# Kernel tuning notes

Measured on AMD Instinct MI355X. Metric: run time of the kernel, lower is better.

## Reference

```python
import jax, jax.numpy as jnp
import numpy as np

N, C, H, M = 4096, 1024, 16, 4096
D = C // H
EPS = 1e-6


def rms_norm(x, g):
    # RMSNorm32: normalize in fp32 with eps=1e-6, affine scale g
    x32 = x.astype(jnp.float32)
    inv = jax.lax.rsqrt(jnp.mean(x32 * x32, axis=-1, keepdims=True) + EPS)
    return (x32 * inv).astype(x.dtype) * g


def setup_inputs() -> dict:
    key = jax.random.key(0)
    ks = jax.random.split(key, 6)
    s = 1.0 / np.sqrt(C)
    return {
        "x": jax.random.normal(ks[0], (N, C), jnp.float32),
        "g1": jnp.ones((C,), jnp.float32),
        "g2": jnp.ones((C,), jnp.float32),
        "w_qkv": jax.random.normal(ks[1], (C, 3 * C), jnp.float32) * s,
        "w_o": jax.random.normal(ks[2], (C, C), jnp.float32) * s,
        "w1": jax.random.normal(ks[3], (C, M), jnp.float32) * s,
        "w2": jax.random.normal(ks[4], (M, C), jnp.float32) * (1.0 / np.sqrt(M)),
    }


def reference(x, g1, g2, w_qkv, w_o, w1, w2):
    # --- pre-norm + full multi-head self-attention over all N sparse tokens ---
    h = rms_norm(x, g1)                                   # [N, C]
    qkv = (h @ w_qkv).reshape(N, 3, H, D)                 # [N, 3, H, D]
    q, k, v = qkv[:, 0], qkv[:, 1], qkv[:, 2]             # [N, H, D]
    scale = 1.0 / np.sqrt(D)
    scores = jnp.einsum('nhd,mhd->hnm', q, k) * scale     # [H, N, N]
    attn = jax.nn.softmax(scores, axis=-1)
    o = jnp.einsum('hnm,mhd->nhd', attn, v).reshape(N, C) # [N, C]
    x = x + o @ w_o                                       # residual
    # --- pre-norm + gated-free MLP (GELU tanh) ---
    h2 = rms_norm(x, g2)
    m = jax.nn.gelu(h2 @ w1, approximate=True) @ w2       # [N, C]
    return x + m
```

## Files before the change

### kernel.cpp

```cpp
#include <hip/hip_runtime.h>
#include <stdint.h>

#define TOK 4096
#define CH  1024
#define NH  16
#define HD  64
#define FF  4096

typedef __attribute__((ext_vector_type(8))) short bf16x8;
typedef __attribute__((ext_vector_type(4))) float f32x4;
typedef __attribute__((ext_vector_type(16))) float f32x16;

__device__ __forceinline__ unsigned short f2bf(float f) {
    union { float f; unsigned u; } v; v.f = f;
    unsigned u = v.u;
    u += 0x7fffu + ((u >> 16) & 1u);
    return (unsigned short)(u >> 16);
}

__device__ __forceinline__ unsigned cvtpk(float a, float b) {
    unsigned r;
    asm("v_cvt_pk_bf16_f32 %0, %1, %2" : "=v"(r) : "v"(a), "v"(b));
    return r;
}

__device__ __forceinline__ void load_lds16(const void* g, void* l) {
    __builtin_amdgcn_global_load_lds(
        (const __attribute__((address_space(1))) unsigned int*)g,
        (__attribute__((address_space(3))) unsigned int*)l, 16, 0, 0);
}

__device__ __forceinline__ float gelu_tanh(float u) {
    float z = 0.7978845608028654f * (u + 0.044715f * u * u * u);
    float e = __expf(2.0f * z);
    return 0.5f * u * (1.0f + (1.0f - 2.0f / (e + 1.0f)));
}

__global__ __launch_bounds__(256) void wT_kernel(const float* __restrict__ in,
                                                 unsigned short* __restrict__ out,
                                                 int K, int Nn) {
    __shared__ float tile[32][33];
    int k0 = blockIdx.x * 32, n0 = blockIdx.y * 32;
    int t = threadIdx.x, r = t >> 3, c = t & 7;
#pragma unroll
    for (int i = 0; i < 4; i++)
        tile[r][c + 8 * i] = in[(size_t)(k0 + r) * Nn + n0 + c + 8 * i];
    __syncthreads();
#pragma unroll
    for (int i = 0; i < 4; i++)
        out[(size_t)(n0 + r) * K + k0 + c + 8 * i] = f2bf(tile[c + 8 * i][r]);
}

__global__ __launch_bounds__(256) void rms_kernel(const float* __restrict__ x,
                                                  const float* __restrict__ g,
                                                  unsigned short* __restrict__ out) {
    int row = blockIdx.x, t = threadIdx.x;
    const float4* xr = (const float4*)(x + (size_t)row * CH);
    float4 v = xr[t];
    float ss = v.x * v.x + v.y * v.y + v.z * v.z + v.w * v.w;
#pragma unroll
    for (int m = 32; m; m >>= 1) ss += __shfl_xor(ss, m, 64);
    __shared__ float wsum[4];
    if ((t & 63) == 0) wsum[t >> 6] = ss;
    __syncthreads();
    float inv = rsqrtf((wsum[0] + wsum[1] + wsum[2] + wsum[3]) * (1.0f / CH) + 1e-6f);
    float4 gv = ((const float4*)g)[t];
    ushort4 o;
    o.x = f2bf(v.x * inv * gv.x);
    o.y = f2bf(v.y * inv * gv.y);
    o.z = f2bf(v.z * inv * gv.z);
    o.w = f2bf(v.w * inv * gv.w);
    ((ushort4*)(out + (size_t)row * CH))[t] = o;
}

template<int BM, int BN, int EPI>
__global__ __launch_bounds__(256) void gemm_bt(const unsigned short* __restrict__ A,
                                               const unsigned short* __restrict__ Bt,
                                               void* __restrict__ outp,
                                               const float* __restrict__ resid,
                                               int M, int Nn, int K) {
    __shared__ __align__(16) unsigned short ldsA[2][BM * 32];
    __shared__ __align__(16) unsigned short ldsB[2][BN * 32];
    const int t = threadIdx.x, l = t & 63, w = t >> 6;
    const int nbn = Nn / BN;
    const int bid = blockIdx.x, nwg = gridDim.x, cpx = nwg >> 3;
    const int swz = (bid & 7) * cpx + (bid >> 3);
    const int bm = swz / nbn, bn = swz % nbn;
    const int wr = w >> 1, wc = w & 1;
    constexpr int MF = BM / 32, NF = BN / 32;
    const unsigned short* Ag = A + (size_t)bm * BM * K;
    const unsigned short* Bg = Bt + (size_t)bn * BN * K;

    f32x4 acc[MF][NF];
#pragma unroll
    for (int m = 0; m < MF; m++)
#pragma unroll
        for (int n = 0; n < NF; n++) acc[m][n] = {0.f, 0.f, 0.f, 0.f};

    auto stage = [&](int buf, int kt) {
#pragma unroll
        for (int p = 0; p < BM / 64; p++) {
            int c = t + 256 * p;
            load_lds16(Ag + (size_t)(c >> 2) * K + kt * 32 + (c & 3) * 8, &ldsA[buf][c * 8]);
        }
#pragma unroll
        for (int p = 0; p < BN / 64; p++) {
            int c = t + 256 * p;
            load_lds16(Bg + (size_t)(c >> 2) * K + kt * 32 + (c & 3) * 8, &ldsB[buf][c * 8]);
        }
    };

    stage(0, 0);
    __syncthreads();
    const int nkt = K >> 5;
    for (int kt = 0; kt < nkt; kt++) {
        const int buf = kt & 1;
        if (kt + 1 < nkt) stage(buf ^ 1, kt + 1);
        bf16x8 af[MF], bfr[NF];
#pragma unroll
        for (int m = 0; m < MF; m++)
            af[m] = *(const bf16x8*)&ldsA[buf][(wr * (BM / 2) + m * 16 + (l & 15)) * 32 + (l >> 4) * 8];
#pragma unroll
        for (int n = 0; n < NF; n++)
            bfr[n] = *(const bf16x8*)&ldsB[buf][(wc * (BN / 2) + n * 16 + (l & 15)) * 32 + (l >> 4) * 8];
#pragma unroll
        for (int m = 0; m < MF; m++)
#pragma unroll
            for (int n = 0; n < NF; n++)
                acc[m][n] = __builtin_amdgcn_mfma_f32_16x16x32_bf16(af[m], bfr[n], acc[m][n], 0, 0, 0);
        __syncthreads();
    }

    const int r0 = bm * BM + wr * (BM / 2), c0 = bn * BN + wc * (BN / 2);
#pragma unroll
    for (int m = 0; m < MF; m++)
#pragma unroll
        for (int n = 0; n < NF; n++)
#pragma unroll
            for (int r = 0; r < 4; r++) {
                int rr = r0 + m * 16 + (l >> 4) * 4 + r;
                int cc = c0 + n * 16 + (l & 15);
                float v = acc[m][n][r];
                if (EPI == 0) {
                    ((unsigned short*)outp)[(size_t)rr * Nn + cc] = f2bf(v);
                } else if (EPI == 1) {
                    ((unsigned short*)outp)[(size_t)rr * Nn + cc] = f2bf(gelu_tanh(v));
                } else if (EPI == 3) {
                    float sc = (cc < 1024) ? 0.180336880f : 1.0f;
                    ((unsigned short*)outp)[(size_t)rr * Nn + cc] = f2bf(v * sc);
                } else {
                    ((float*)outp)[(size_t)rr * Nn + cc] = resid[(size_t)rr * Nn + cc] + v;
                }
            }
}

__global__ __launch_bounds__(256) void vT_kernel(const unsigned short* __restrict__ qkv,
                                                 unsigned short* __restrict__ vT) {
    __shared__ unsigned short tile[64][80];
    const int t = threadIdx.x;
    const int t0 = blockIdx.x * 64;
    const int h = blockIdx.y;
#pragma unroll
    for (int p = 0; p < 2; p++) {
        int c = t + 256 * p;
        int r = c >> 3, c8 = (c & 7) * 8;
        bf16x8 v = *(const bf16x8*)(qkv + (size_t)(t0 + r) * 3072 + 2048 + h * 64 + c8);
        *(bf16x8*)&tile[r][c8] = v;
    }
    __syncthreads();
#pragma unroll
    for (int p = 0; p < 2; p++) {
        int c = t + 256 * p;
        int col = c >> 3, r8 = (c & 7) * 8;
        union { unsigned short u[8]; bf16x8 v; } o;
#pragma unroll
        for (int j = 0; j < 8; j++) o.u[j] = tile[r8 + j][col];
        *(bf16x8*)(vT + (size_t)(h * 64 + col) * 4096 + t0 + r8) = o.v;
    }
}

__global__ __launch_bounds__(256) void attn_kernel(const unsigned short* __restrict__ qkv,
                                                   const unsigned short* __restrict__ vT,
                                                   unsigned short* __restrict__ o) {
    __shared__ __align__(16) unsigned short Kl[2][4096];
    __shared__ __align__(16) unsigned short Vl[2][4096];
    const int t = threadIdx.x, l = t & 63, w = t >> 6;
    const int h = blockIdx.y;
    const int qrow = blockIdx.x * 128 + w * 32 + (l & 31);

    bf16x8 qf[4];
    {
        const unsigned short* qp = qkv + (size_t)qrow * 3072 + h * 64 + ((l >> 5) * 8);
#pragma unroll
        for (int c = 0; c < 4; c++) qf[c] = *(const bf16x8*)(qp + 16 * c);
    }
    const unsigned short* kb = qkv + 1024 + h * 64;
    const unsigned short* vb = vT + (size_t)h * 64 * 4096;

    int off8[4];
#pragma unroll
    for (int c = 0; c < 4; c++)
        off8[c] = (l & 31) * 64 + ((((l >> 5) + 2 * c) ^ (l & 7)) * 8);
    int kst[2], vst[2];
#pragma unroll
    for (int p = 0; p < 2; p++) {
        int c = t + 256 * p;
        int r = c >> 3, b = c & 7;
        kst[p] = r * 3072 + ((b ^ (r & 7)) * 8);
        vst[p] = r * 4096 + ((b ^ (r & 7)) * 8);
    }

    float lrun = 0.f;
    const f32x16 z16 = {0.f, 0.f, 0.f, 0.f, 0.f, 0.f, 0.f, 0.f,
                        0.f, 0.f, 0.f, 0.f, 0.f, 0.f, 0.f, 0.f};
    f32x16 accO[2];
#pragma unroll
    for (int dt = 0; dt < 2; dt++) accO[dt] = z16;

    auto stage = [&](int buf, int kt) {
#pragma unroll
        for (int p = 0; p < 2; p++)
            load_lds16(kb + (size_t)kt * 64 * 3072 + kst[p], &Kl[buf][(t + 256 * p) * 8]);
#pragma unroll
        for (int p = 0; p < 2; p++)
            load_lds16(vb + kt * 64 + vst[p], &Vl[buf][(t + 256 * p) * 8]);
    };

    stage(0, 0);
    __syncthreads();

    for (int kt = 0; kt < 64; kt++) {
        const int cur = kt & 1;
        if (kt + 1 < 64) stage(cur ^ 1, kt + 1);

        f32x16 s[2];
        __builtin_amdgcn_s_setprio(1);
#pragma unroll
        for (int st = 0; st < 2; st++) {
            bf16x8 kf0 = *(const bf16x8*)&Kl[cur][st * 2048 + off8[0]];
            s[st] = __builtin_amdgcn_mfma_f32_32x32x16_bf16(kf0, qf[0], z16, 0, 0, 0);
#pragma unroll
            for (int c = 1; c < 4; c++) {
                bf16x8 kf = *(const bf16x8*)&Kl[cur][st * 2048 + off8[c]];
                s[st] = __builtin_amdgcn_mfma_f32_32x32x16_bf16(kf, qf[c], s[st], 0, 0, 0);
            }
        }
        __builtin_amdgcn_s_setprio(0);

        float rs = 0.f;
#pragma unroll
        for (int st = 0; st < 2; st++)
#pragma unroll
            for (int i = 0; i < 16; i++) {
                float p = __builtin_amdgcn_exp2f(s[st][i]);
                s[st][i] = p;
                rs += p;
            }
        lrun += rs;

#pragma unroll
        for (int kc = 0; kc < 4; kc++) {
            const int base = 8 * (kc & 1);
            const f32x16& S = s[kc >> 1];
            unsigned w0 = cvtpk(S[base + 0], S[base + 1]);
            unsigned w1 = cvtpk(S[base + 2], S[base + 3]);
            unsigned w2 = cvtpk(S[base + 4], S[base + 5]);
            unsigned w3 = cvtpk(S[base + 6], S[base + 7]);
            asm("v_permlane32_swap_b32 %0, %1" : "+v"(w0), "+v"(w2));
            asm("v_permlane32_swap_b32 %0, %1" : "+v"(w1), "+v"(w3));
            union { unsigned u[4]; bf16x8 v; } pf;
            pf.u[0] = w0; pf.u[1] = w1; pf.u[2] = w2; pf.u[3] = w3;
            __builtin_amdgcn_s_setprio(1);
#pragma unroll
            for (int dt = 0; dt < 2; dt++) {
                bf16x8 vf = *(const bf16x8*)&Vl[cur][dt * 2048 + off8[kc]];
                accO[dt] = __builtin_amdgcn_mfma_f32_32x32x16_bf16(vf, pf.v, accO[dt], 0, 0, 0);
            }
            __builtin_amdgcn_s_setprio(0);
        }
        __syncthreads();
    }

    lrun += __shfl_xor(lrun, 32, 64);
    float inv = 1.0f / lrun;
    unsigned short* ob = o + (size_t)qrow * CH + h * 64 + 4 * (l >> 5);
#pragma unroll
    for (int dt = 0; dt < 2; dt++)
#pragma unroll
        for (int qd = 0; qd < 4; qd++) {
            ushort4 pk;
            pk.x = f2bf(accO[dt][qd * 4 + 0] * inv);
            pk.y = f2bf(accO[dt][qd * 4 + 1] * inv);
            pk.z = f2bf(accO[dt][qd * 4 + 2] * inv);
            pk.w = f2bf(accO[dt][qd * 4 + 3] * inv);
            *(ushort4*)(ob + dt * 32 + qd * 8) = pk;
        }
}

extern "C" void kernel_launch(void* const* d_in, const int* in_sizes, int n_in,
                              void* d_out, int out_size, void* d_ws, size_t ws_size,
                              hipStream_t stream) {
    const float* x     = (const float*)d_in[0];
    const float* g1    = (const float*)d_in[1];
    const float* g2    = (const float*)d_in[2];
    const float* w_qkv = (const float*)d_in[3];
    const float* w_o   = (const float*)d_in[4];
    const float* w1    = (const float*)d_in[5];
    const float* w2    = (const float*)d_in[6];

    char* ws = (char*)d_ws;
    unsigned short* wqkvT = (unsigned short*)(ws);
    unsigned short* woT   = (unsigned short*)(ws + 6291456);
    unsigned short* w1T   = (unsigned short*)(ws + 8388608);
    unsigned short* w2T   = (unsigned short*)(ws + 16777216);
    unsigned short* hbuf  = (unsigned short*)(ws + 25165824);
    unsigned short* qkv   = (unsigned short*)(ws + 33554432);
    unsigned short* obuf  = (unsigned short*)(ws + 58720256);
    float*          x2    = (float*)(ws + 67108864);
    unsigned short* abuf  = (unsigned short*)(ws + 83886080);
    unsigned short* vTb   = (unsigned short*)(ws + 83886080);

    dim3 b256(256);
    wT_kernel<<<dim3(CH / 32, 3 * CH / 32), b256, 0, stream>>>(w_qkv, wqkvT, CH, 3 * CH);
    wT_kernel<<<dim3(CH / 32, CH / 32),     b256, 0, stream>>>(w_o,   woT,   CH, CH);
    wT_kernel<<<dim3(CH / 32, FF / 32),     b256, 0, stream>>>(w1,    w1T,   CH, FF);
    wT_kernel<<<dim3(FF / 32, CH / 32),     b256, 0, stream>>>(w2,    w2T,   FF, CH);

    rms_kernel<<<TOK, b256, 0, stream>>>(x, g1, hbuf);
    gemm_bt<128, 128, 3><<<(TOK / 128) * (3 * CH / 128), b256, 0, stream>>>(hbuf, wqkvT, qkv, nullptr, TOK, 3 * CH, CH);
    vT_kernel<<<dim3(TOK / 64, NH), b256, 0, stream>>>(qkv, vTb);
    attn_kernel<<<dim3(TOK / 128, NH), b256, 0, stream>>>(qkv, vTb, obuf);
    gemm_bt<64, 128, 2><<<(TOK / 64) * (CH / 128), b256, 0, stream>>>(obuf, woT, x2, x, TOK, CH, CH);
    rms_kernel<<<TOK, b256, 0, stream>>>(x2, g2, hbuf);
    gemm_bt<128, 128, 1><<<(TOK / 128) * (FF / 128), b256, 0, stream>>>(hbuf, w1T, abuf, nullptr, TOK, FF, CH);
    gemm_bt<64, 128, 2><<<(TOK / 64) * (CH / 128), b256, 0, stream>>>(abuf, w2T, (float*)d_out, x2, TOK, CH, FF);
}
```

Baseline: 313.4 us.

## Triple-buffer LDS staging with partial vmcnt waits in GEMM and attention

```diff
diff --git a/kernel.cpp b/kernel.cpp
--- a/kernel.cpp
+++ b/kernel.cpp
@@ -28,6 +28,14 @@
     __builtin_amdgcn_global_load_lds(
         (const __attribute__((address_space(1))) unsigned int*)g,
         (__attribute__((address_space(3))) unsigned int*)l, 16, 0, 0);
+}
+
+template<int N> __device__ __forceinline__ void wait_vm_lgkm0() {
+    if constexpr (N == 0)      asm volatile("s_waitcnt vmcnt(0) lgkmcnt(0)" ::: "memory");
+    else if constexpr (N == 3) asm volatile("s_waitcnt vmcnt(3) lgkmcnt(0)" ::: "memory");
+    else if constexpr (N == 4) asm volatile("s_waitcnt vmcnt(4) lgkmcnt(0)" ::: "memory");
+    __builtin_amdgcn_sched_barrier(0);
+    __builtin_amdgcn_s_barrier();
 }
 
 __device__ __forceinline__ float gelu_tanh(float u) {
@@ -79,8 +87,9 @@
                                                void* __restrict__ outp,
                                                const float* __restrict__ resid,
                                                int M, int Nn, int K) {
-    __shared__ __align__(16) unsigned short ldsA[2][BM * 32];
-    __shared__ __align__(16) unsigned short ldsB[2][BN * 32];
+    __shared__ __align__(16) unsigned short ldsA[3][BM * 32];
+    __shared__ __align__(16) unsigned short ldsB[3][BN * 32];
+    constexpr int LPS = BM / 64 + BN / 64;
     const int t = threadIdx.x, l = t & 63, w = t >> 6;
     const int nbn = Nn / BN;
     const int bid = blockIdx.x, nwg = gridDim.x, cpx = nwg >> 3;
@@ -110,12 +119,14 @@
         }
     };
 
+    const int nkt = K >> 5;
     stage(0, 0);
-    __syncthreads();
-    const int nkt = K >> 5;
+    stage(1, 1);
+    wait_vm_lgkm0<LPS>();
+
     for (int kt = 0; kt < nkt; kt++) {
-        const int buf = kt & 1;
-        if (kt + 1 < nkt) stage(buf ^ 1, kt + 1);
+        const int buf = kt % 3;
+        if (kt + 2 < nkt) stage((kt + 2) % 3, kt + 2);
         bf16x8 af[MF], bfr[NF];
 #pragma unroll
         for (int m = 0; m < MF; m++)
@@ -128,7 +139,10 @@
 #pragma unroll
             for (int n = 0; n < NF; n++)
                 acc[m][n] = __builtin_amdgcn_mfma_f32_16x16x32_bf16(af[m], bfr[n], acc[m][n], 0, 0, 0);
-        __syncthreads();
+        if (kt + 1 < nkt) {
+            if (kt + 2 < nkt) wait_vm_lgkm0<LPS>();
+            else              wait_vm_lgkm0<0>();
+        }
     }
 
     const int r0 = bm * BM + wr * (BM / 2), c0 = bn * BN + wc * (BN / 2);
@@ -182,8 +196,8 @@
 __global__ __launch_bounds__(256) void attn_kernel(const unsigned short* __restrict__ qkv,
                                                    const unsigned short* __restrict__ vT,
                                                    unsigned short* __restrict__ o) {
-    __shared__ __align__(16) unsigned short Kl[2][4096];
-    __shared__ __align__(16) unsigned short Vl[2][4096];
+    __shared__ __align__(16) unsigned short Kl[3][4096];
+    __shared__ __align__(16) unsigned short Vl[3][4096];
     const int t = threadIdx.x, l = t & 63, w = t >> 6;
     const int h = blockIdx.y;
     const int qrow = blockIdx.x * 128 + w * 32 + (l & 31);
@@ -227,11 +241,12 @@
     };
 
     stage(0, 0);
-    __syncthreads();
+    stage(1, 1);
+    wait_vm_lgkm0<4>();
 
     for (int kt = 0; kt < 64; kt++) {
-        const int cur = kt & 1;
-        if (kt + 1 < 64) stage(cur ^ 1, kt + 1);
+        const int cur = kt % 3;
+        if (kt + 2 < 64) stage((kt + 2) % 3, kt + 2);
 
         f32x16 s[2];
         __builtin_amdgcn_s_setprio(1);
@@ -278,7 +293,11 @@
             }
             __builtin_amdgcn_s_setprio(0);
         }
-        __syncthreads();
+
+        if (kt < 63) {
+            if (kt + 2 < 64) wait_vm_lgkm0<4>();
+            else             wait_vm_lgkm0<0>();
+        }
     }
 
     lrun += __shfl_xor(lrun, 32, 64);
```

After: 325.3 us. 1.04x slower.
